# Performance work log

Hardware: AMD Instinct MI355X
Metric: run time of the kernel (lower is better)

The kernel has to match this reference:

```python
import jax, jax.numpy as jnp
import numpy as np
from jax import lax

EPS = 1e-4

def whatever_norm(z):
    m = jnp.mean(z, axis=-1, keepdims=True)
    v = jnp.var(z, axis=-1, keepdims=True)
    return (z - m) * lax.rsqrt(v + EPS)

def attend_layer(x_seq, speech, Ua_W, Ua_b, Wa_W, Wa_b, va_W, va_b, K, R, b):
    # x_seq: [B, T, U], speech: [B, Te, E]
    B = x_seq.shape[0]
    units = R.shape[0]
    enc = speech @ Ua_W + Ua_b  # [B, Te, U]  (Ua(speech_encode))

    def step(carry, x_t):
        h, c = carry
        s = h @ Wa_W + Wa_b                                   # Wa(states[0]) [B,U]
        logits = jnp.squeeze(jnp.tanh(s[:, None, :] + enc) @ va_W + va_b, -1)  # [B,Te]
        w = jax.nn.softmax(logits, axis=-1)
        ctx = jnp.einsum('bt,bte->be', w, speech)             # context [B,E]
        z = jnp.concatenate([x_t, ctx], axis=1) @ K + h @ R + b
        i, f, g, o = jnp.split(z, 4, axis=1)                  # keras gate order i,f,c,o
        i = jax.nn.sigmoid(i); f = jax.nn.sigmoid(f); o = jax.nn.sigmoid(o)
        c_new = f * c + i * jnp.tanh(g)
        h_new = o * jnp.tanh(c_new)
        return (h_new, c_new), h_new

    h0 = jnp.zeros((B, units), x_seq.dtype)
    _, ys = lax.scan(step, (h0, h0), jnp.swapaxes(x_seq, 0, 1))
    return jnp.swapaxes(ys, 0, 1)  # [B, T, U]


def setup_inputs() -> dict:
    key = jax.random.key(0)
    ks = iter(jax.random.split(key, 40))
    B, Td, Te, E, U, NC = 64, 512, 1024, 512, 256, 64
    g = lambda *s: (jax.random.normal(next(ks), s, dtype=jnp.float32) * (1.0 / np.sqrt(s[0])))
    inp = {
        'trans': jax.random.normal(next(ks), (B, Td, NC), dtype=jnp.float32),
        'speech': jax.random.normal(next(ks), (B, Te, E), dtype=jnp.float32),
        'emb_W': g(NC, U), 'emb_b': jnp.zeros((U,), jnp.float32),
    }
    for L in ('1', '2'):
        inp['Ua%s_W' % L] = g(E, U); inp['Ua%s_b' % L] = jnp.zeros((U,), jnp.float32)
        inp['Wa%s_W' % L] = g(U, U); inp['Wa%s_b' % L] = jnp.zeros((U,), jnp.float32)
        inp['va%s_W' % L] = g(U, 1); inp['va%s_b' % L] = jnp.zeros((1,), jnp.float32)
        inp['K%s' % L] = g(U + E, 4 * U)
        inp['R%s' % L] = g(U, 4 * U)
        # bias_initializer_two_cell: zeros for i, 2.0 for f, zeros for c and o
        inp['b%s' % L] = jnp.concatenate([
            jnp.zeros((U,)), 2.0 * jnp.ones((U,)), jnp.zeros((2 * U,))]).astype(jnp.float32)
    inp['m1_W'] = g(U, U); inp['m1_b'] = jnp.zeros((U,), jnp.float32)
    inp['m2_W'] = g(U, U); inp['m2_b'] = jnp.zeros((U,), jnp.float32)
    inp['d_W'] = g(U, NC); inp['d_b'] = jnp.zeros((NC,), jnp.float32)
    return inp


def reference(trans, speech, emb_W, emb_b,
              Ua1_W, Ua1_b, Wa1_W, Wa1_b, va1_W, va1_b, K1, R1, b1,
              Ua2_W, Ua2_b, Wa2_W, Wa2_b, va2_W, va2_b, K2, R2, b2,
              m1_W, m1_b, m2_W, m2_b, d_W, d_b):
    secrets = trans @ emb_W + emb_b
    out = attend_layer(secrets, speech, Ua1_W, Ua1_b, Wa1_W, Wa1_b, va1_W, va1_b, K1, R1, b1)
    out = whatever_norm(out)
    out = attend_layer(out, speech, Ua2_W, Ua2_b, Wa2_W, Wa2_b, va2_W, va2_b, K2, R2, b2)
    out = whatever_norm(out)
    out = whatever_norm(out @ m1_W + m1_b)
    out = whatever_norm(out @ m2_W + m2_b)
    return jax.nn.softmax(out @ d_W + d_b, axis=-1)
```

## Files before the change

### kernel.cpp

```cpp
#include <hip/hip_runtime.h>
#include <hip/hip_bf16.h>
#include <stdint.h>

#define B  64
#define TD 512
#define TE 1024
#define EE 512
#define UU 256

__device__ __forceinline__ float fexp2(float x){ return __builtin_amdgcn_exp2f(x); }
__device__ __forceinline__ float frcp_(float x){ return __builtin_amdgcn_rcpf(x); }
__device__ __forceinline__ float tanh_fast(float x){
  float e = fexp2(x * 2.885390082f);
  return 1.f - 2.f * frcp_(e + 1.f);
}
__device__ __forceinline__ float sigmoid_fast(float x){
  return frcp_(1.f + fexp2(-1.442695041f * x));
}
__device__ __forceinline__ unsigned short f2bf(float f){
  unsigned int u = __float_as_uint(f);
  u = (u + 0x7fffu + ((u >> 16) & 1u)) >> 16;
  return (unsigned short)u;
}
__device__ __forceinline__ float bflo(unsigned int w){ return __uint_as_float(w << 16); }
__device__ __forceinline__ float bfhi(unsigned int w){ return __uint_as_float(w & 0xffff0000u); }

__device__ __forceinline__ void gstore(float* p, float v){
  __hip_atomic_store(p, v, __ATOMIC_RELAXED, __HIP_MEMORY_SCOPE_SYSTEM);
}
__device__ __forceinline__ float gload(const float* p){
  return __hip_atomic_load(p, __ATOMIC_RELAXED, __HIP_MEMORY_SCOPE_SYSTEM);
}
__device__ __forceinline__ void drain_stores(){
  __atomic_signal_fence(__ATOMIC_SEQ_CST);
  __builtin_amdgcn_s_waitcnt(0);
  __atomic_signal_fence(__ATOMIC_SEQ_CST);
}

__global__ void pack_bf16v(const float* __restrict__ in, unsigned short* __restrict__ out, int n4){
  int i = blockIdx.x * blockDim.x + threadIdx.x;
  int stride = gridDim.x * blockDim.x;
  for (; i < n4; i += stride){
    float4 v = ((const float4*)in)[i];
    ushort4 o;
    o.x = f2bf(v.x); o.y = f2bf(v.y); o.z = f2bf(v.z); o.w = f2bf(v.w);
    ((ushort4*)out)[i] = o;
  }
}

__global__ void pack_KRP(const float* __restrict__ K, const float* __restrict__ R,
                         unsigned short* __restrict__ KRP){
  int idx = blockIdx.x * 256 + threadIdx.x;
  int q  = idx >> 18;
  int k  = (idx >> 8) & 1023;
  int jj = idx & 255;
  int J  = (jj >> 6)*256 + q*64 + (jj & 63);
  float v = (k < 768) ? K[(size_t)k*1024 + J] : R[(size_t)(k - 768)*1024 + J];
  KRP[idx] = f2bf(v);
}

__global__ __launch_bounds__(256) void emb_gemm(const float* __restrict__ trans,
    const float* __restrict__ W, const float* __restrict__ bias, float* __restrict__ out){
  __shared__ __align__(16) float aT[64*20];
  const int row0 = blockIdx.x * 16;
  const int tid = threadIdx.x;
  {
    int r = tid >> 6, k = tid & 63;
    for (int rr = r; rr < 16; rr += 4)
      aT[k*20 + rr] = trans[(size_t)(row0 + rr)*64 + k];
  }
  __syncthreads();
  const int j = tid;
  float bj = bias[j];
  float acc[16];
  #pragma unroll
  for (int r = 0; r < 16; ++r) acc[r] = bj;
  for (int k = 0; k < 64; ++k){
    float w = W[(size_t)k*UU + j];
    const float4* a4 = (const float4*)(aT + k*20);
    float4 q0 = a4[0], q1 = a4[1], q2 = a4[2], q3 = a4[3];
    acc[0]+=q0.x*w;  acc[1]+=q0.y*w;  acc[2]+=q0.z*w;  acc[3]+=q0.w*w;
    acc[4]+=q1.x*w;  acc[5]+=q1.y*w;  acc[6]+=q1.z*w;  acc[7]+=q1.w*w;
    acc[8]+=q2.x*w;  acc[9]+=q2.y*w;  acc[10]+=q2.z*w; acc[11]+=q2.w*w;
    acc[12]+=q3.x*w; acc[13]+=q3.y*w; acc[14]+=q3.z*w; acc[15]+=q3.w*w;
  }
  #pragma unroll
  for (int r = 0; r < 16; ++r)
    out[(size_t)(row0 + r)*UU + j] = acc[r];
}

__global__ __launch_bounds__(256) void enc_gemm(const float* __restrict__ speech,
    const float* __restrict__ Ua, const float* __restrict__ Uab,
    unsigned short* __restrict__ enc){
  __shared__ __align__(16) float aT[512*20];
  const int wg = blockIdx.x;
  const int b = wg >> 6, tb = (wg & 63) * 16;
  const int tid = threadIdx.x;
  const float* sp = speech + ((size_t)b*TE + tb)*EE;
  for (int it = 0; it < 32; ++it){
    int idx = tid + 256*it;
    int te = idx >> 9, e = idx & 511;
    aT[e*20 + te] = sp[(size_t)te*EE + e];
  }
  __syncthreads();
  const int j = tid;
  float bj = Uab[j];
  float acc[16];
  #pragma unroll
  for (int r = 0; r < 16; ++r) acc[r] = bj;
  const float* up = Ua + j;
  for (int e = 0; e < 512; ++e){
    float w = up[(size_t)e*UU];
    const float4* a4 = (const float4*)(aT + e*20);
    float4 q0 = a4[0], q1 = a4[1], q2 = a4[2], q3 = a4[3];
    acc[0]+=q0.x*w;  acc[1]+=q0.y*w;  acc[2]+=q0.z*w;  acc[3]+=q0.w*w;
    acc[4]+=q1.x*w;  acc[5]+=q1.y*w;  acc[6]+=q1.z*w;  acc[7]+=q1.w*w;
    acc[8]+=q2.x*w;  acc[9]+=q2.y*w;  acc[10]+=q2.z*w; acc[11]+=q2.w*w;
    acc[12]+=q3.x*w; acc[13]+=q3.y*w; acc[14]+=q3.z*w; acc[15]+=q3.w*w;
  }
  unsigned short* op = enc + ((size_t)b*TE + tb)*UU + j;
  #pragma unroll
  for (int r = 0; r < 16; ++r) op[(size_t)r*UU] = f2bf(acc[r]);
}

__global__ __launch_bounds__(1024) void scan_kernel(
    const float* __restrict__ x_seq, float* __restrict__ y_out,
    const unsigned short* __restrict__ enc, const unsigned short* __restrict__ speech,
    const unsigned short* __restrict__ KRP, const unsigned short* __restrict__ Wab,
    const float* __restrict__ Wa_b, const float* __restrict__ va,
    const float* __restrict__ gate_b,
    float* __restrict__ pctx_g, float* __restrict__ l_g, float* __restrict__ h_g,
    unsigned int* __restrict__ ctr){
  extern __shared__ __align__(16) unsigned short enc_l[];
  __shared__ float2 sva[256];
  __shared__ float cat[1024];
  __shared__ float c_lds[64];
  __shared__ float lds_logit[256];
  __shared__ float p_lds[256];
  __shared__ float lds_pctx[512];
  __shared__ float lds_z[256];
  __shared__ float s_acc[256];
  __shared__ float red[32];
  __shared__ float nmi[2];

  const int tid = threadIdx.x;
  const int wg = blockIdx.x;
  const int b = wg >> 2, q = wg & 3;
  const int lane = tid & 63, wave = tid >> 6;
  unsigned int bar = 0;
  unsigned int* cptr = &ctr[b*16];

  {
    const uint4* ep4 = (const uint4*)(enc + ((size_t)b*TE + q*256)*UU);
    #pragma unroll
    for (int i = 0; i < 8; ++i){
      int idx = tid + 1024*i;
      int te_l = idx >> 5, ch = idx & 31;
      uint4 v = ep4[(size_t)te_l*32 + ch];
      *(uint4*)(enc_l + (size_t)te_l*264 + ch*8) = v;
    }
  }
  if (tid < 256){ sva[tid] = make_float2(Wa_b[tid], va[tid]); cat[768 + tid] = 0.f; }
  if (tid < 64) c_lds[tid] = 0.f;
  __syncthreads();

  for (int t = 0; t < TD; ++t){
    if (tid < 256){ lds_logit[tid] = 0.f; lds_z[tid] = 0.f; s_acc[tid] = 0.f; }
    if (tid < 512) lds_pctx[tid] = 0.f;
    __syncthreads();

    {
      const int g = wave & 3, r = wave >> 2;
      const int te_l = g*64 + lane;
      const unsigned short* ep = enc_l + (size_t)te_l*264 + r*64;
      float acc = 0.f;
      #pragma unroll
      for (int c = 0; c < 8; ++c){
        uint4 v = *(const uint4*)(ep + c*8);
        const int ub = r*64 + c*8;
        unsigned int wv[4] = {v.x, v.y, v.z, v.w};
        #pragma unroll
        for (int i = 0; i < 4; ++i){
          float2 s0 = sva[ub + 2*i];
          float2 s1 = sva[ub + 2*i + 1];
          acc += s0.y * tanh_fast(s0.x + bflo(wv[i]));
          acc += s1.y * tanh_fast(s1.x + bfhi(wv[i]));
        }
      }
      atomicAdd(&lds_logit[te_l], acc);
    }
    __syncthreads();

    if (tid < 256){
      float p = fexp2(lds_logit[tid] * 1.442695041f);
      p_lds[tid] = p;
      float s = p;
      #pragma unroll
      for (int o = 32; o > 0; o >>= 1) s += __shfl_xor(s, o);
      if (lane == 0) red[wave] = s;
    }
    __syncthreads();

    {
      const int c = tid & 63, tg = tid >> 6;
      const uint4* sp4 = (const uint4*)speech + ((size_t)b*TE + q*256 + tg*16)*64 + c;
      float a0=0.f,a1=0.f,a2=0.f,a3=0.f,a4=0.f,a5=0.f,a6=0.f,a7=0.f;
      #pragma unroll 4
      for (int i = 0; i < 16; ++i){
        uint4 w = sp4[(size_t)i*64];
        float p = p_lds[tg*16 + i];
        a0 += p*bflo(w.x); a1 += p*bfhi(w.x);
        a2 += p*bflo(w.y); a3 += p*bfhi(w.y);
        a4 += p*bflo(w.z); a5 += p*bfhi(w.z);
        a6 += p*bflo(w.w); a7 += p*bfhi(w.w);
      }
      atomicAdd(&lds_pctx[c*8+0], a0); atomicAdd(&lds_pctx[c*8+1], a1);
      atomicAdd(&lds_pctx[c*8+2], a2); atomicAdd(&lds_pctx[c*8+3], a3);
      atomicAdd(&lds_pctx[c*8+4], a4); atomicAdd(&lds_pctx[c*8+5], a5);
      atomicAdd(&lds_pctx[c*8+6], a6); atomicAdd(&lds_pctx[c*8+7], a7);
    }
    __syncthreads();
    if (tid < 512) gstore(&pctx_g[((size_t)(b*4 + q))*512 + tid], lds_pctx[tid]);
    if (tid == 0)  gstore(&l_g[b*4 + q], red[0] + red[1] + red[2] + red[3]);
    drain_stores();
    __syncthreads();
    bar += 4;
    if (tid == 0){
      __hip_atomic_fetch_add(cptr, 1u, __ATOMIC_RELAXED, __HIP_MEMORY_SCOPE_SYSTEM);
      while (__hip_atomic_load(cptr, __ATOMIC_RELAXED, __HIP_MEMORY_SCOPE_SYSTEM) < bar)
        __builtin_amdgcn_s_sleep(2);
    }
    __syncthreads();

    if (tid < 512){
      float l0 = gload(&l_g[b*4+0]), l1 = gload(&l_g[b*4+1]);
      float l2 = gload(&l_g[b*4+2]), l3 = gload(&l_g[b*4+3]);
      float linv = frcp_(l0 + l1 + l2 + l3);
      float s0 = gload(&pctx_g[((size_t)(b*4+0))*512 + tid])
               + gload(&pctx_g[((size_t)(b*4+1))*512 + tid])
               + gload(&pctx_g[((size_t)(b*4+2))*512 + tid])
               + gload(&pctx_g[((size_t)(b*4+3))*512 + tid]);
      cat[256 + tid] = s0 * linv;
    } else if (tid < 768){
      const int u = tid - 512;
      cat[u] = x_seq[((size_t)b*TD + t)*UU + u];
    }
    __syncthreads();

    {
      const int c = tid & 31, kg = tid >> 5;
      const uint4* kp = (const uint4*)KRP + ((size_t)q*1024 + kg*32)*32 + c;
      float a0=0.f,a1=0.f,a2=0.f,a3=0.f,a4=0.f,a5=0.f,a6=0.f,a7=0.f;
      #pragma unroll 4
      for (int i = 0; i < 32; ++i){
        uint4 w = kp[(size_t)i*32];
        float ck = cat[kg*32 + i];
        a0 += ck*bflo(w.x); a1 += ck*bfhi(w.x);
        a2 += ck*bflo(w.y); a3 += ck*bfhi(w.y);
        a4 += ck*bflo(w.z); a5 += ck*bfhi(w.z);
        a6 += ck*bflo(w.w); a7 += ck*bfhi(w.w);
      }
      a0 += __shfl_xor(a0, 32); a1 += __shfl_xor(a1, 32);
      a2 += __shfl_xor(a2, 32); a3 += __shfl_xor(a3, 32);
      a4 += __shfl_xor(a4, 32); a5 += __shfl_xor(a5, 32);
      a6 += __shfl_xor(a6, 32); a7 += __shfl_xor(a7, 32);
      if (lane < 32){
        atomicAdd(&lds_z[c*8+0], a0); atomicAdd(&lds_z[c*8+1], a1);
        atomicAdd(&lds_z[c*8+2], a2); atomicAdd(&lds_z[c*8+3], a3);
        atomicAdd(&lds_z[c*8+4], a4); atomicAdd(&lds_z[c*8+5], a5);
        atomicAdd(&lds_z[c*8+6], a6); atomicAdd(&lds_z[c*8+7], a7);
      }
    }
    __syncthreads();

    if (tid < 64){
      const int jj = q*64 + tid;
      float zi = lds_z[tid]       + gate_b[jj];
      float zf = lds_z[64 + tid]  + gate_b[256 + jj];
      float zg = lds_z[128 + tid] + gate_b[512 + jj];
      float zo = lds_z[192 + tid] + gate_b[768 + jj];
      float cn = sigmoid_fast(zf) * c_lds[tid] + sigmoid_fast(zi) * tanh_fast(zg);
      c_lds[tid] = cn;
      gstore(&h_g[(size_t)b*UU + jj], sigmoid_fast(zo) * tanh_fast(cn));
    }
    drain_stores();
    __syncthreads();
    bar += 4;
    if (tid == 0){
      __hip_atomic_fetch_add(cptr, 1u, __ATOMIC_RELAXED, __HIP_MEMORY_SCOPE_SYSTEM);
      while (__hip_atomic_load(cptr, __ATOMIC_RELAXED, __HIP_MEMORY_SCOPE_SYSTEM) < bar)
        __builtin_amdgcn_s_sleep(2);
    }
    __syncthreads();

    if (tid < 256) cat[768 + tid] = gload(&h_g[(size_t)b*UU + tid]);
    __syncthreads();

    if (q == 0){
      if (tid < 256){
        float hv = cat[768 + tid];
        float s1 = hv, s2 = hv*hv;
        #pragma unroll
        for (int o = 32; o > 0; o >>= 1){ s1 += __shfl_xor(s1, o); s2 += __shfl_xor(s2, o); }
        if (lane == 0){ red[wave*2] = s1; red[wave*2 + 1] = s2; }
      }
      __syncthreads();
      if (tid == 0){
        float m  = (red[0] + red[2] + red[4] + red[6]) * (1.f/256.f);
        float ms = (red[1] + red[3] + red[5] + red[7]) * (1.f/256.f);
        nmi[0] = m;
        nmi[1] = rsqrtf(ms - m*m + 1e-4f);
      }
      __syncthreads();
      if (tid < 256)
        y_out[((size_t)b*TD + t)*UU + tid] = (cat[768 + tid] - nmi[0]) * nmi[1];
    }

    if (t < TD - 1){
      {
        const int c = tid & 31, kg = tid >> 5;
        const uint4* wp = (const uint4*)Wab + (size_t)(kg*8)*32 + c;
        float a0=0.f,a1=0.f,a2=0.f,a3=0.f,a4=0.f,a5=0.f,a6=0.f,a7=0.f;
        #pragma unroll 4
        for (int i = 0; i < 8; ++i){
          uint4 w = wp[(size_t)i*32];
          float hk = cat[768 + kg*8 + i];
          a0 += hk*bflo(w.x); a1 += hk*bfhi(w.x);
          a2 += hk*bflo(w.y); a3 += hk*bfhi(w.y);
          a4 += hk*bflo(w.z); a5 += hk*bfhi(w.z);
          a6 += hk*bflo(w.w); a7 += hk*bfhi(w.w);
        }
        a0 += __shfl_xor(a0, 32); a1 += __shfl_xor(a1, 32);
        a2 += __shfl_xor(a2, 32); a3 += __shfl_xor(a3, 32);
        a4 += __shfl_xor(a4, 32); a5 += __shfl_xor(a5, 32);
        a6 += __shfl_xor(a6, 32); a7 += __shfl_xor(a7, 32);
        if (lane < 32){
          atomicAdd(&s_acc[c*8+0], a0); atomicAdd(&s_acc[c*8+1], a1);
          atomicAdd(&s_acc[c*8+2], a2); atomicAdd(&s_acc[c*8+3], a3);
          atomicAdd(&s_acc[c*8+4], a4); atomicAdd(&s_acc[c*8+5], a5);
          atomicAdd(&s_acc[c*8+6], a6); atomicAdd(&s_acc[c*8+7], a7);
        }
      }
      __syncthreads();
      if (tid < 256) sva[tid].x = Wa_b[tid] + s_acc[tid];
    }
    __syncthreads();
  }
}

__global__ __launch_bounds__(256) void head_kernel(const float* __restrict__ y2,
    const float* __restrict__ m1W, const float* __restrict__ m1b,
    const float* __restrict__ m2W, const float* __restrict__ m2b,
    const float* __restrict__ dW, const float* __restrict__ db,
    float* __restrict__ out){
  __shared__ __align__(16) float aT[256*20];
  __shared__ float t_lds[16*256];
  __shared__ float zl[16*64];
  __shared__ float mi[32];
  const int row0 = blockIdx.x * 16;
  const int tid = threadIdx.x;
  for (int it = 0; it < 16; ++it){
    int idx = tid + 256*it;
    int r = idx >> 8, k = idx & 255;
    aT[k*20 + r] = y2[(size_t)(row0 + r)*UU + k];
  }
  __syncthreads();

  #pragma unroll 1
  for (int pass = 0; pass < 2; ++pass){
    const float* Wp = pass ? m2W : m1W;
    const float* bp = pass ? m2b : m1b;
    const int j = tid;
    float bj = bp[j];
    float acc[16];
    #pragma unroll
    for (int r = 0; r < 16; ++r) acc[r] = bj;
    for (int k = 0; k < 256; ++k){
      float w = Wp[(size_t)k*UU + j];
      const float4* a4 = (const float4*)(aT + k*20);
      float4 q0 = a4[0], q1 = a4[1], q2 = a4[2], q3 = a4[3];
      acc[0]+=q0.x*w;  acc[1]+=q0.y*w;  acc[2]+=q0.z*w;  acc[3]+=q0.w*w;
      acc[4]+=q1.x*w;  acc[5]+=q1.y*w;  acc[6]+=q1.z*w;  acc[7]+=q1.w*w;
      acc[8]+=q2.x*w;  acc[9]+=q2.y*w;  acc[10]+=q2.z*w; acc[11]+=q2.w*w;
      acc[12]+=q3.x*w; acc[13]+=q3.y*w; acc[14]+=q3.z*w; acc[15]+=q3.w*w;
    }
    #pragma unroll
    for (int r = 0; r < 16; ++r) t_lds[r*256 + j] = acc[r];
    __syncthreads();
    {
      int r = tid >> 4, sg = tid & 15;
      float s1 = 0.f, s2 = 0.f;
      for (int c = 0; c < 16; ++c){
        float v = t_lds[r*256 + sg*16 + c];
        s1 += v; s2 += v*v;
      }
      for (int o = 1; o < 16; o <<= 1){ s1 += __shfl_xor(s1, o); s2 += __shfl_xor(s2, o); }
      if (sg == 0){
        float m = s1 * (1.f/256.f);
        float vv = s2 * (1.f/256.f) - m*m;
        mi[r*2] = m; mi[r*2+1] = rsqrtf(vv + 1e-4f);
      }
    }
    __syncthreads();
    {
      const int j2 = tid;
      #pragma unroll
      for (int r = 0; r < 16; ++r)
        aT[j2*20 + r] = (t_lds[r*256 + j2] - mi[r*2]) * mi[r*2+1];
    }
    __syncthreads();
  }

  for (int i = tid; i < 1024; i += 256) zl[i] = 0.f;
  __syncthreads();
  {
    const int j = tid & 63, kq = tid >> 6;
    float acc[16];
    #pragma unroll
    for (int r = 0; r < 16; ++r) acc[r] = 0.f;
    for (int k = 0; k < 64; ++k){
      float w = dW[(size_t)(kq*64 + k)*64 + j];
      const float4* a4 = (const float4*)(aT + (kq*64 + k)*20);
      float4 q0 = a4[0], q1 = a4[1], q2 = a4[2], q3 = a4[3];
      acc[0]+=q0.x*w;  acc[1]+=q0.y*w;  acc[2]+=q0.z*w;  acc[3]+=q0.w*w;
      acc[4]+=q1.x*w;  acc[5]+=q1.y*w;  acc[6]+=q1.z*w;  acc[7]+=q1.w*w;
      acc[8]+=q2.x*w;  acc[9]+=q2.y*w;  acc[10]+=q2.z*w; acc[11]+=q2.w*w;
      acc[12]+=q3.x*w; acc[13]+=q3.y*w; acc[14]+=q3.z*w; acc[15]+=q3.w*w;
    }
    #pragma unroll
    for (int r = 0; r < 16; ++r) atomicAdd(&zl[r*64 + j], acc[r]);
  }
  __syncthreads();
  if (tid < 16){
    const int r = tid;
    float mx = -1e30f;
    for (int j = 0; j < 64; ++j){ float v = zl[r*64 + j] + db[j]; zl[r*64 + j] = v; mx = fmaxf(mx, v); }
    float s = 0.f;
    for (int j = 0; j < 64; ++j){ float e = fexp2((zl[r*64 + j] - mx) * 1.442695041f); zl[r*64 + j] = e; s += e; }
    mi[r] = frcp_(s);
  }
  __syncthreads();
  for (int it = 0; it < 4; ++it){
    int idx = tid + 256*it;
    int r = idx >> 6, j = idx & 63;
    out[(size_t)(row0 + r)*64 + j] = zl[r*64 + j] * mi[r];
  }
}

#define OFF_SPEECH 0u
#define OFF_ENC    67108864u
#define OFF_KR     100663296u
#define OFF_WA     102760448u
#define OFF_X1     102891520u
#define OFF_Y1     136445952u
#define OFF_PCTX   170000384u
#define OFF_L      170524672u
#define OFF_H      170528768u
#define OFF_CTR    170594304u

#define DYN_LDS    135168

extern "C" void kernel_launch(void* const* d_in, const int* in_sizes, int n_in,
                              void* d_out, int out_size, void* d_ws, size_t ws_size,
                              hipStream_t stream){
  const float* trans  = (const float*)d_in[0];
  const float* speech = (const float*)d_in[1];
  const float* emb_W  = (const float*)d_in[2];
  const float* emb_b  = (const float*)d_in[3];
  const float* Ua_W[2]  = {(const float*)d_in[4],  (const float*)d_in[13]};
  const float* Ua_b[2]  = {(const float*)d_in[5],  (const float*)d_in[14]};
  const float* Wa_W[2]  = {(const float*)d_in[6],  (const float*)d_in[15]};
  const float* Wa_bv[2] = {(const float*)d_in[7],  (const float*)d_in[16]};
  const float* va_W[2]  = {(const float*)d_in[8],  (const float*)d_in[17]};
  const float* Kw[2]    = {(const float*)d_in[10], (const float*)d_in[19]};
  const float* Rw[2]    = {(const float*)d_in[11], (const float*)d_in[20]};
  const float* bw[2]    = {(const float*)d_in[12], (const float*)d_in[21]};
  const float* m1W = (const float*)d_in[22];
  const float* m1b = (const float*)d_in[23];
  const float* m2W = (const float*)d_in[24];
  const float* m2b = (const float*)d_in[25];
  const float* dW  = (const float*)d_in[26];
  const float* db  = (const float*)d_in[27];

  char* ws = (char*)d_ws;
  unsigned short* speech_bf = (unsigned short*)(ws + OFF_SPEECH);
  unsigned short* enc  = (unsigned short*)(ws + OFF_ENC);
  unsigned short* KRP  = (unsigned short*)(ws + OFF_KR);
  unsigned short* Wab  = (unsigned short*)(ws + OFF_WA);
  float* x1   = (float*)(ws + OFF_X1);
  float* y1   = (float*)(ws + OFF_Y1);
  float* pctx = (float*)(ws + OFF_PCTX);
  float* lg   = (float*)(ws + OFF_L);
  float* hg   = (float*)(ws + OFF_H);
  unsigned int* ctr = (unsigned int*)(ws + OFF_CTR);
  float* y2 = x1;

  hipFuncSetAttribute((const void*)scan_kernel,
                      hipFuncAttributeMaxDynamicSharedMemorySize, DYN_LDS);

  hipMemsetAsync(ctr, 0, 4096, stream);
  pack_bf16v<<<4096, 256, 0, stream>>>(speech, speech_bf, B*TE*EE/4);
  emb_gemm<<<2048, 256, 0, stream>>>(trans, emb_W, emb_b, x1);

  for (int L = 0; L < 2; ++L){
    enc_gemm<<<4096, 256, 0, stream>>>(speech, Ua_W[L], Ua_b[L], enc);
    pack_KRP<<<4096, 256, 0, stream>>>(Kw[L], Rw[L], KRP);
    pack_bf16v<<<64, 256, 0, stream>>>(Wa_W[L], Wab, UU*UU/4);
    if (L == 1) hipMemsetAsync(ctr, 0, 4096, stream);
    scan_kernel<<<256, 1024, DYN_LDS, stream>>>(L == 0 ? x1 : y1, L == 0 ? y1 : y2,
        enc, speech_bf, KRP, Wab, Wa_bv[L], va_W[L], bw[L], pctx, lg, hg, ctr);
  }

  head_kernel<<<2048, 256, 0, stream>>>(y2, m1W, m1b, m2W, m2b, dW, db, (float*)d_out);
  (void)in_sizes; (void)n_in; (void)out_size; (void)ws_size;
}
```

Before: 40.86 ms.

## Overlap gate matvec pieces with inter-block barrier waits and prefetch weights

Splits the barrier into arrive and wait so each block does useful gate work while the other blocks of the same batch catch up. The x_t part of the gate matvec for the next step and the h part for the current step run during those waits, with double-buffered z accumulators. The block also prefetches the context-part weights into registers. Attention logits are written into four per-row partial buffers instead of LDS atomics. This adds register pressure and more complex buffer indexing.

```diff
diff --git a/kernel.cpp b/kernel.cpp
--- a/kernel.cpp
+++ b/kernel.cpp
@@ -35,6 +35,33 @@
   __atomic_signal_fence(__ATOMIC_SEQ_CST);
   __builtin_amdgcn_s_waitcnt(0);
   __atomic_signal_fence(__ATOMIC_SEQ_CST);
+}
+
+template<int NITER>
+__device__ __forceinline__ void gate_accum(const unsigned short* __restrict__ KRP,
+    const float* catp, float* zb, int q, int k0, int tid, int lane){
+  const int c = tid & 31, kg = tid >> 5;
+  const uint4* kp = (const uint4*)KRP + ((size_t)q*1024 + k0 + kg*NITER)*32 + c;
+  float a0=0.f,a1=0.f,a2=0.f,a3=0.f,a4=0.f,a5=0.f,a6=0.f,a7=0.f;
+  #pragma unroll 4
+  for (int i = 0; i < NITER; ++i){
+    uint4 w = kp[(size_t)i*32];
+    float ck = catp[k0 + kg*NITER + i];
+    a0 += ck*bflo(w.x); a1 += ck*bfhi(w.x);
+    a2 += ck*bflo(w.y); a3 += ck*bfhi(w.y);
+    a4 += ck*bflo(w.z); a5 += ck*bfhi(w.z);
+    a6 += ck*bflo(w.w); a7 += ck*bfhi(w.w);
+  }
+  a0 += __shfl_xor(a0, 32); a1 += __shfl_xor(a1, 32);
+  a2 += __shfl_xor(a2, 32); a3 += __shfl_xor(a3, 32);
+  a4 += __shfl_xor(a4, 32); a5 += __shfl_xor(a5, 32);
+  a6 += __shfl_xor(a6, 32); a7 += __shfl_xor(a7, 32);
+  if (lane < 32){
+    atomicAdd(&zb[c*8+0], a0); atomicAdd(&zb[c*8+1], a1);
+    atomicAdd(&zb[c*8+2], a2); atomicAdd(&zb[c*8+3], a3);
+    atomicAdd(&zb[c*8+4], a4); atomicAdd(&zb[c*8+5], a5);
+    atomicAdd(&zb[c*8+6], a6); atomicAdd(&zb[c*8+7], a7);
+  }
 }
 
 __global__ void pack_bf16v(const float* __restrict__ in, unsigned short* __restrict__ out, int n4){
@@ -135,10 +162,10 @@
   __shared__ float2 sva[256];
   __shared__ float cat[1024];
   __shared__ float c_lds[64];
-  __shared__ float lds_logit[256];
+  __shared__ float lds_logit4[1024];
   __shared__ float p_lds[256];
   __shared__ float lds_pctx[512];
-  __shared__ float lds_z[256];
+  __shared__ float zbuf[2][256];
   __shared__ float s_acc[256];
   __shared__ float red[32];
   __shared__ float nmi[2];
@@ -160,13 +187,20 @@
       *(uint4*)(enc_l + (size_t)te_l*264 + ch*8) = v;
     }
   }
-  if (tid < 256){ sva[tid] = make_float2(Wa_b[tid], va[tid]); cat[768 + tid] = 0.f; }
+  if (tid < 256){ sva[tid] = make_float2(Wa_b[tid], va[tid]); cat[768 + tid] = 0.f;
+                  zbuf[0][tid] = 0.f; zbuf[1][tid] = 0.f; }
   if (tid < 64) c_lds[tid] = 0.f;
-  __syncthreads();
+  if (tid >= 512 && tid < 768)
+    cat[tid - 512] = x_seq[((size_t)b*TD + 0)*UU + (tid - 512)];
+  __syncthreads();
+  gate_accum<8>(KRP, cat, zbuf[0], q, 0, tid, lane);
 
   for (int t = 0; t < TD; ++t){
-    if (tid < 256){ lds_logit[tid] = 0.f; lds_z[tid] = 0.f; s_acc[tid] = 0.f; }
     if (tid < 512) lds_pctx[tid] = 0.f;
+    if (tid < 256){ zbuf[(t+1)&1][tid] = 0.f; s_acc[tid] = 0.f; }
+    float xnext = 0.f;
+    if (t < TD-1 && tid >= 512 && tid < 768)
+      xnext = x_seq[((size_t)b*TD + t + 1)*UU + (tid - 512)];
     __syncthreads();
 
     {
@@ -187,12 +221,14 @@
           acc += s1.y * tanh_fast(s1.x + bfhi(wv[i]));
         }
       }
-      atomicAdd(&lds_logit[te_l], acc);
+      lds_logit4[r*256 + te_l] = acc;
     }
     __syncthreads();
 
     if (tid < 256){
-      float p = fexp2(lds_logit[tid] * 1.442695041f);
+      float lg = lds_logit4[tid] + lds_logit4[256 + tid]
+               + lds_logit4[512 + tid] + lds_logit4[768 + tid];
+      float p = fexp2(lg * 1.442695041f);
       p_lds[tid] = p;
       float s = p;
       #pragma unroll
@@ -225,8 +261,20 @@
     drain_stores();
     __syncthreads();
     bar += 4;
+    if (tid == 0)
+      __hip_atomic_fetch_add(cptr, 1u, __ATOMIC_RELAXED, __HIP_MEMORY_SCOPE_SYSTEM);
+
+    gate_accum<8>(KRP, cat, zbuf[t&1], q, 768, tid, lane);
+
+    uint4 pf[8];
+    {
+      const int c = tid & 31, kg = tid >> 5;
+      const uint4* kp = (const uint4*)KRP + ((size_t)q*1024 + 256 + kg*16)*32 + c;
+      #pragma unroll
+      for (int i = 0; i < 8; ++i) pf[i] = kp[(size_t)i*32];
+    }
+
     if (tid == 0){
-      __hip_atomic_fetch_add(cptr, 1u, __ATOMIC_RELAXED, __HIP_MEMORY_SCOPE_SYSTEM);
       while (__hip_atomic_load(cptr, __ATOMIC_RELAXED, __HIP_MEMORY_SCOPE_SYSTEM) < bar)
         __builtin_amdgcn_s_sleep(2);
     }
@@ -241,53 +289,67 @@
                + gload(&pctx_g[((size_t)(b*4+2))*512 + tid])
                + gload(&pctx_g[((size_t)(b*4+3))*512 + tid]);
       cat[256 + tid] = s0 * linv;
-    } else if (tid < 768){
-      const int u = tid - 512;
-      cat[u] = x_seq[((size_t)b*TD + t)*UU + u];
     }
     __syncthreads();
 
     {
       const int c = tid & 31, kg = tid >> 5;
-      const uint4* kp = (const uint4*)KRP + ((size_t)q*1024 + kg*32)*32 + c;
+      const uint4* kp = (const uint4*)KRP + ((size_t)q*1024 + 256 + kg*16)*32 + c;
       float a0=0.f,a1=0.f,a2=0.f,a3=0.f,a4=0.f,a5=0.f,a6=0.f,a7=0.f;
-      #pragma unroll 4
-      for (int i = 0; i < 32; ++i){
-        uint4 w = kp[(size_t)i*32];
-        float ck = cat[kg*32 + i];
+      #pragma unroll
+      for (int i = 0; i < 8; ++i){
+        uint4 w = pf[i];
+        float ck = cat[256 + kg*16 + i];
         a0 += ck*bflo(w.x); a1 += ck*bfhi(w.x);
         a2 += ck*bflo(w.y); a3 += ck*bfhi(w.y);
         a4 += ck*bflo(w.z); a5 += ck*bfhi(w.z);
         a6 += ck*bflo(w.w); a7 += ck*bfhi(w.w);
       }
+      #pragma unroll 4
+      for (int i = 8; i < 16; ++i){
+        uint4 w = kp[(size_t)i*32];
+        float ck = cat[256 + kg*16 + i];
+        a0 += ck*bflo(w.x); a1 += ck*bfhi(w.x);
+        a2 += ck*bflo(w.y); a3 += ck*bfhi(w.y);
+        a4 += ck*bflo(w.z); a5 += ck*bfhi(w.z);
+        a6 += ck*bflo(w.w); a7 += ck*bfhi(w.w);
+      }
       a0 += __shfl_xor(a0, 32); a1 += __shfl_xor(a1, 32);
       a2 += __shfl_xor(a2, 32); a3 += __shfl_xor(a3, 32);
       a4 += __shfl_xor(a4, 32); a5 += __shfl_xor(a5, 32);
       a6 += __shfl_xor(a6, 32); a7 += __shfl_xor(a7, 32);
+      float* zb = zbuf[t&1];
       if (lane < 32){
-        atomicAdd(&lds_z[c*8+0], a0); atomicAdd(&lds_z[c*8+1], a1);
-        atomicAdd(&lds_z[c*8+2], a2); atomicAdd(&lds_z[c*8+3], a3);
-        atomicAdd(&lds_z[c*8+4], a4); atomicAdd(&lds_z[c*8+5], a5);
-        atomicAdd(&lds_z[c*8+6], a6); atomicAdd(&lds_z[c*8+7], a7);
+        atomicAdd(&zb[c*8+0], a0); atomicAdd(&zb[c*8+1], a1);
+        atomicAdd(&zb[c*8+2], a2); atomicAdd(&zb[c*8+3], a3);
+        atomicAdd(&zb[c*8+4], a4); atomicAdd(&zb[c*8+5], a5);
+        atomicAdd(&zb[c*8+6], a6); atomicAdd(&zb[c*8+7], a7);
       }
     }
     __syncthreads();
 
     if (tid < 64){
       const int jj = q*64 + tid;
-      float zi = lds_z[tid]       + gate_b[jj];
-      float zf = lds_z[64 + tid]  + gate_b[256 + jj];
-      float zg = lds_z[128 + tid] + gate_b[512 + jj];
-      float zo = lds_z[192 + tid] + gate_b[768 + jj];
+      const float* zb = zbuf[t&1];
+      float zi = zb[tid]       + gate_b[jj];
+      float zf = zb[64 + tid]  + gate_b[256 + jj];
+      float zg = zb[128 + tid] + gate_b[512 + jj];
+      float zo = zb[192 + tid] + gate_b[768 + jj];
       float cn = sigmoid_fast(zf) * c_lds[tid] + sigmoid_fast(zi) * tanh_fast(zg);
       c_lds[tid] = cn;
       gstore(&h_g[(size_t)b*UU + jj], sigmoid_fast(zo) * tanh_fast(cn));
     }
+    if (t < TD-1 && tid >= 512 && tid < 768) cat[tid - 512] = xnext;
     drain_stores();
     __syncthreads();
     bar += 4;
+    if (tid == 0)
+      __hip_atomic_fetch_add(cptr, 1u, __ATOMIC_RELAXED, __HIP_MEMORY_SCOPE_SYSTEM);
+
+    if (t < TD-1)
+      gate_accum<8>(KRP, cat, zbuf[(t+1)&1], q, 0, tid, lane);
+
     if (tid == 0){
-      __hip_atomic_fetch_add(cptr, 1u, __ATOMIC_RELAXED, __HIP_MEMORY_SCOPE_SYSTEM);
       while (__hip_atomic_load(cptr, __ATOMIC_RELAXED, __HIP_MEMORY_SCOPE_SYSTEM) < bar)
         __builtin_amdgcn_s_sleep(2);
     }
```

After: 66.91 ms. 63.7% more time.
